# Kernel tuning notes

Measured on AMD Instinct MI355X. Metric: run time of the kernel, lower is better.

Reference implementation:

```python
import math
import jax, jax.numpy as jnp
import numpy as np

B, C, H, W = 8, 512, 32, 32
N_HEADS = 8
N_GROUPS = 32  # GroupNorm(32) as in guided-diffusion normalization()
EPS = 1e-5


def setup_inputs() -> dict:
    key = jax.random.key(0)
    k0, k1, k2, k3, k4 = jax.random.split(key, 5)
    x = jax.random.normal(k0, (B, C, H, W), dtype=jnp.float32)
    gn_scale = jnp.ones((C,), dtype=jnp.float32)
    gn_bias = jnp.zeros((C,), dtype=jnp.float32)
    # 1x1 conv weights stored as (out, in); proj_out is zero-initialized in the
    # original but we use small random weights so the op is non-trivial.
    qkv_w = jax.random.normal(k1, (3 * C, C), dtype=jnp.float32) * 0.02
    qkv_b = jax.random.normal(k2, (3 * C,), dtype=jnp.float32) * 0.02
    proj_w = jax.random.normal(k3, (C, C), dtype=jnp.float32) * 0.02
    proj_b = jax.random.normal(k4, (C,), dtype=jnp.float32) * 0.02
    return {"x": x, "gn_scale": gn_scale, "gn_bias": gn_bias,
            "qkv_w": qkv_w, "qkv_b": qkv_b, "proj_w": proj_w, "proj_b": proj_b}


def reference(x, gn_scale, gn_bias, qkv_w, qkv_b, proj_w, proj_b):
    b, c, h, w = x.shape
    L = h * w
    xf = x.reshape(b, c, L)

    # GroupNorm(32): normalize over (channels-in-group, length)
    xg = xf.reshape(b, N_GROUPS, c // N_GROUPS, L)
    mu = jnp.mean(xg, axis=(2, 3), keepdims=True)
    var = jnp.var(xg, axis=(2, 3), keepdims=True)
    xn = ((xg - mu) * jax.lax.rsqrt(var + EPS)).reshape(b, c, L)
    xn = xn * gn_scale[None, :, None] + gn_bias[None, :, None]

    # 1x1 conv -> qkv (b, 3c, L)
    qkv = jnp.einsum('oc,bcl->bol', qkv_w, xn) + qkv_b[None, :, None]

    ch = c // N_HEADS  # head dim (width//(3*n_heads) of qkv)
    q, k, v = jnp.split(qkv, 3, axis=1)
    q = q.reshape(b * N_HEADS, ch, L)
    k = k.reshape(b * N_HEADS, ch, L)
    v = v.reshape(b * N_HEADS, ch, L)

    scale = 1.0 / math.sqrt(math.sqrt(ch))
    # scores: (b*heads, L, L) materialized, as in the original
    wts = jnp.einsum('bct,bcs->bts', q * scale, k * scale)
    wts = jax.nn.softmax(wts.astype(jnp.float32), axis=-1).astype(q.dtype)
    a = jnp.einsum('bts,bcs->bct', wts, v).reshape(b, c, L)

    # zero-initialized 1x1 proj in original; random weights here
    hout = jnp.einsum('oc,bcl->bol', proj_w, a) + proj_b[None, :, None]
    return (xf + hout).reshape(b, c, h, w)
```

## Files before the change

kernel.cpp:

```cpp
#include <hip/hip_runtime.h>
#include <math.h>

#define BATCH   8
#define CCH     512
#define LL      1024
#define NHEADS  8
#define CHD     64
#define EPSV    1e-5f
#define QSCALE  0.1803368801111204f

typedef __bf16 bf16_t;
typedef bf16_t bf16x8 __attribute__((ext_vector_type(8)));
typedef bf16_t bf16x4 __attribute__((ext_vector_type(4)));
typedef float  f32x4  __attribute__((ext_vector_type(4)));

__device__ __forceinline__ bf16_t f2b(float f) {
  unsigned u = __float_as_uint(f);
  u += 0x7fff + ((u >> 16) & 1);
  return __builtin_bit_cast(bf16_t, (unsigned short)(u >> 16));
}

__device__ __forceinline__ unsigned pack2(float lo, float hi) {
  unsigned a = (unsigned)__builtin_bit_cast(unsigned short, f2b(lo));
  unsigned b = (unsigned)__builtin_bit_cast(unsigned short, f2b(hi));
  return (b << 16) | a;
}

__device__ __forceinline__ void gload_lds16(const void* g, void* l) {
  __builtin_amdgcn_global_load_lds(
      (const __attribute__((address_space(1))) void*)g,
      (__attribute__((address_space(3))) void*)l, 16, 0, 0);
}

__global__ __launch_bounds__(256) void prep_fused(const float* __restrict__ qkvw,
                                                  const float* __restrict__ projw,
                                                  bf16_t* __restrict__ wqb,
                                                  bf16_t* __restrict__ wpb,
                                                  const float* __restrict__ x,
                                                  const float* __restrict__ gsc,
                                                  const float* __restrict__ gbi,
                                                  bf16_t* __restrict__ xnT) {
  int bid = blockIdx.x;
  int tid = threadIdx.x;
  if (bid < 1024) {
    int i = (bid * 256 + tid) * 4;
    const float* src;
    bf16_t* dst;
    int j;
    if (i < 1536 * 512) { src = qkvw; dst = wqb; j = i; }
    else                { src = projw; dst = wpb; j = i - 1536 * 512; }
    float4 v = *(const float4*)(src + j);
    bf16x4 o = {f2b(v.x), f2b(v.y), f2b(v.z), f2b(v.w)};
    *(bf16x4*)(dst + j) = o;
    return;
  }
  int lin = bid - 1024;
  int xcd = lin & 7, slot = lin >> 3;
  int b = slot & 7, jj = slot >> 3;
  int g = xcd * 4 + jj;
  const float4* x4 = (const float4*)(x + ((size_t)(b * 32 + g)) * 16 * LL);

  float s = 0.f, ss = 0.f;
  float4 v[16];
#pragma unroll
  for (int it = 0; it < 16; ++it) {
    float4 f = x4[it * 256 + tid];
    v[it] = f;
    s += f.x + f.y + f.z + f.w;
    ss += f.x * f.x + f.y * f.y + f.z * f.z + f.w * f.w;
  }
#pragma unroll
  for (int m = 1; m < 64; m <<= 1) { s += __shfl_xor(s, m); ss += __shfl_xor(ss, m); }
  __shared__ float rs_[4], rss[4];
  int wv = tid >> 6, ln = tid & 63;
  if (ln == 0) { rs_[wv] = s; rss[wv] = ss; }
  __syncthreads();
  s  = rs_[0] + rs_[1] + rs_[2] + rs_[3];
  ss = rss[0] + rss[1] + rss[2] + rss[3];
  float mean = s * (1.f / 16384.f);
  float var  = ss * (1.f / 16384.f) - mean * mean;
  float rstd = rsqrtf(var + EPSV);

  float sc[16], bi[16];
#pragma unroll
  for (int it = 0; it < 16; ++it) {
    sc[it] = gsc[g * 16 + it] * rstd;
    bi[it] = gbi[g * 16 + it] - mean * sc[it];
  }

#pragma unroll
  for (int j = 0; j < 4; ++j) {
    unsigned w[8];
#pragma unroll
    for (int k = 0; k < 8; ++k) {
      float a0 = (j == 0 ? v[2 * k].x : j == 1 ? v[2 * k].y : j == 2 ? v[2 * k].z : v[2 * k].w);
      float a1 = (j == 0 ? v[2 * k + 1].x : j == 1 ? v[2 * k + 1].y : j == 2 ? v[2 * k + 1].z : v[2 * k + 1].w);
      w[k] = pack2(a0 * sc[2 * k] + bi[2 * k], a1 * sc[2 * k + 1] + bi[2 * k + 1]);
    }
    int l = tid * 4 + j;
    bf16_t* dst = xnT + ((size_t)b * LL + l) * CCH + g * 16;
    *(uint4*)dst = make_uint4(w[0], w[1], w[2], w[3]);
    *(uint4*)(dst + 8) = make_uint4(w[4], w[5], w[6], w[7]);
  }
}

__global__ __launch_bounds__(256, 2) void qkv_mfma(const bf16_t* __restrict__ wq,
                                                   const bf16_t* __restrict__ xnT,
                                                   const float* __restrict__ qkvb,
                                                   bf16_t* __restrict__ qt,
                                                   bf16_t* __restrict__ kt,
                                                   bf16_t* __restrict__ vt) {
  __shared__ bf16_t As[128 * 64];
  __shared__ bf16_t Bs[256 * 64];
  int tid = threadIdx.x;
  int wave = tid >> 6, lane = tid & 63;
  int lrow = lane & 15, quad = lane >> 4;
  int wm = wave >> 1, wn = wave & 1;
  int b = blockIdx.x;
  int oBase = blockIdx.y * 128, lBase = blockIdx.z * 256;
  int srow = lane >> 3;
  int sgOff = (((lane & 7) ^ srow) << 4);

  f32x4 acc[4][8] = {};
  for (int ktile = 0; ktile < 8; ++ktile) {
    int kB = ktile * 64;
    __syncthreads();
#pragma unroll
    for (int j = 0; j < 4; ++j) {
      int ci = wave * 4 + j;
      int R = ci * 8 + srow;
      gload_lds16((const char*)(wq + (size_t)(oBase + R) * CCH + kB) + sgOff,
                  (char*)As + ci * 1024);
    }
#pragma unroll
    for (int j = 0; j < 8; ++j) {
      int ci = wave * 8 + j;
      int R = ci * 8 + srow;
      gload_lds16((const char*)(xnT + ((size_t)b * LL + lBase + R) * CCH + kB) + sgOff,
                  (char*)Bs + ci * 1024);
    }
    __syncthreads();
#pragma unroll
    for (int kk = 0; kk < 2; ++kk) {
      int g = (kk * 4 + quad) ^ (lrow & 7);
      bf16x8 af[4], bfr[8];
#pragma unroll
      for (int m = 0; m < 4; ++m) {
        int r = wm * 64 + m * 16 + lrow;
        af[m] = *(const bf16x8*)(As + r * 64 + g * 8);
      }
#pragma unroll
      for (int n = 0; n < 8; ++n) {
        int r = wn * 128 + n * 16 + lrow;
        bfr[n] = *(const bf16x8*)(Bs + r * 64 + g * 8);
      }
#pragma unroll
      for (int m = 0; m < 4; ++m)
#pragma unroll
        for (int n = 0; n < 8; ++n)
          acc[m][n] = __builtin_amdgcn_mfma_f32_16x16x32_bf16(af[m], bfr[n], acc[m][n], 0, 0, 0);
    }
  }

  int oW = oBase + wm * 64;
  int lW = lBase + wn * 128;
  int sec = oW >> 9;
#pragma unroll
  for (int m = 0; m < 4; ++m) {
    int o4 = oW + m * 16 + quad * 4;
    float4 bb4 = *(const float4*)&qkvb[o4];
    int cc = o4 & 511;
    int head = cc >> 6, ch = cc & 63;
    int bh = b * NHEADS + head;
    if (sec == 0) {
#pragma unroll
      for (int n = 0; n < 8; ++n) {
        int l = lW + n * 16 + lrow;
        unsigned d0 = pack2((acc[m][n][0] + bb4.x) * QSCALE,
                            (acc[m][n][1] + bb4.y) * QSCALE);
        unsigned d1 = pack2((acc[m][n][2] + bb4.z) * QSCALE,
                            (acc[m][n][3] + bb4.w) * QSCALE);
        *(uint2*)(qt + ((size_t)bh * LL + l) * CHD + ch) = make_uint2(d0, d1);
      }
    } else if (sec == 1) {
#pragma unroll
      for (int n = 0; n < 8; ++n) {
        int l = lW + n * 16 + lrow;
        unsigned d0 = pack2(acc[m][n][0] + bb4.x, acc[m][n][1] + bb4.y);
        unsigned d1 = pack2(acc[m][n][2] + bb4.z, acc[m][n][3] + bb4.w);
        *(uint2*)(kt + ((size_t)bh * LL + l) * CHD + ch) = make_uint2(d0, d1);
      }
    } else {
      float bb[4] = {bb4.x, bb4.y, bb4.z, bb4.w};
#pragma unroll
      for (int c = 0; c < 2; ++c) {
#pragma unroll
        for (int i = 0; i < 4; ++i) {
          unsigned d0 = pack2(acc[m][c * 4 + 0][i] + bb[i], acc[m][c * 4 + 1][i] + bb[i]);
          unsigned d1 = pack2(acc[m][c * 4 + 2][i] + bb[i], acc[m][c * 4 + 3][i] + bb[i]);
          *(uint2*)(vt + ((size_t)bh * CHD + ch + i) * LL + lW + c * 64 + lrow * 4) =
              make_uint2(d0, d1);
        }
      }
    }
  }
}

__global__ __launch_bounds__(256) void attn_mfma(const bf16_t* __restrict__ qt,
                                                 const bf16_t* __restrict__ kt,
                                                 const bf16_t* __restrict__ vt,
                                                 bf16_t* __restrict__ at) {
  __shared__ bf16_t kbuf[2][64 * 64];
  __shared__ bf16_t vbuf[2][64 * 64];
  __shared__ bf16_t pb[8 * 16 * 72];
  int tid = threadIdx.x, wave = tid >> 6, lane = tid & 63;
  int lrow = lane & 15, quad = lane >> 4;
  int bh = blockIdx.x;
  int tW = blockIdx.y * 128 + wave * 32;
  const bf16_t* qb = qt + (size_t)bh * LL * CHD;
  const bf16_t* kb = kt + (size_t)bh * LL * CHD;
  const bf16_t* vb = vt + (size_t)bh * CHD * LL;

  int srow = lane >> 3;
  int sgb = (((lane & 7) ^ srow) << 4);

  bf16x8 qf[2][2];
#pragma unroll
  for (int h = 0; h < 2; ++h) {
    const bf16_t* qp = qb + (size_t)(tW + h * 16 + lrow) * CHD + quad * 8;
    qf[h][0] = *(const bf16x8*)qp;
    qf[h][1] = *(const bf16x8*)(qp + 32);
  }

  bf16x8 ones;
#pragma unroll
  for (int j = 0; j < 8; ++j) ones[j] = (bf16_t)1.0f;

  f32x4 Oa[2][4] = {};
  f32x4 Os[2] = {};

#pragma unroll
  for (int j = 0; j < 2; ++j) {
    int c = wave * 2 + j;
    int R = c * 8 + srow;
    gload_lds16((const char*)(kb + (size_t)R * CHD) + sgb, (char*)&kbuf[0][0] + c * 1024);
    gload_lds16((const char*)(vb + (size_t)R * LL) + sgb, (char*)&vbuf[0][0] + c * 1024);
  }
  __syncthreads();

  int swz0 = (quad ^ (lrow & 7)) * 8;
  int swz1 = ((quad + 4) ^ (lrow & 7)) * 8;

  for (int st = 0; st < 16; ++st) {
    int cur = st & 1;
    if (st < 15) {
      int sBn = (st + 1) * 64;
#pragma unroll
      for (int j = 0; j < 2; ++j) {
        int c = wave * 2 + j;
        int R = c * 8 + srow;
        gload_lds16((const char*)(kb + (size_t)(sBn + R) * CHD) + sgb,
                    (char*)&kbuf[cur ^ 1][0] + c * 1024);
        gload_lds16((const char*)(vb + (size_t)R * LL + sBn) + sgb,
                    (char*)&vbuf[cur ^ 1][0] + c * 1024);
      }
    }
    const bf16_t* kbase = &kbuf[cur][0];
    const bf16_t* vbase = &vbuf[cur][0];

    f32x4 S[2][4];
#pragma unroll
    for (int ss = 0; ss < 4; ++ss) {
      int s = ss * 16 + lrow;
      bf16x8 k0 = *(const bf16x8*)(kbase + s * 64 + swz0);
      bf16x8 k1 = *(const bf16x8*)(kbase + s * 64 + swz1);
#pragma unroll
      for (int h = 0; h < 2; ++h) {
        f32x4 z = {0.f, 0.f, 0.f, 0.f};
        z = __builtin_amdgcn_mfma_f32_16x16x32_bf16(qf[h][0], k0, z, 0, 0, 0);
        S[h][ss] = __builtin_amdgcn_mfma_f32_16x16x32_bf16(qf[h][1], k1, z, 0, 0, 0);
      }
    }

#pragma unroll
    for (int h = 0; h < 2; ++h) {
      bf16_t* pw = pb + (wave * 2 + h) * (16 * 72);
      float p[4][4];
#pragma unroll
      for (int ss = 0; ss < 4; ++ss)
#pragma unroll
        for (int i = 0; i < 4; ++i)
          p[ss][i] = __builtin_amdgcn_exp2f(S[h][ss][i]);
#pragma unroll
      for (int i = 0; i < 4; ++i) {
        unsigned d0 = __builtin_amdgcn_perm(__float_as_uint(p[1][i]),
                                            __float_as_uint(p[0][i]), 0x07060302u);
        unsigned d1 = __builtin_amdgcn_perm(__float_as_uint(p[3][i]),
                                            __float_as_uint(p[2][i]), 0x07060302u);
        uint2* dst = (uint2*)(pw + (quad * 4 + i) * 72 + lrow * 4);
        *dst = make_uint2(d0, d1);
      }
    }
    asm volatile("s_waitcnt lgkmcnt(0)" ::: "memory");

    bf16x8 pf[2][2];
#pragma unroll
    for (int h = 0; h < 2; ++h) {
      const bf16_t* pw = pb + (wave * 2 + h) * (16 * 72);
      pf[h][0] = *(const bf16x8*)(pw + lrow * 72 + quad * 8);
      pf[h][1] = *(const bf16x8*)(pw + lrow * 72 + 32 + quad * 8);
    }

#pragma unroll
    for (int n = 0; n < 4; ++n) {
      int r = (n * 16 + lrow) * 64;
      bf16x8 v0 = *(const bf16x8*)(vbase + r + swz0);
      bf16x8 v1 = *(const bf16x8*)(vbase + r + swz1);
#pragma unroll
      for (int h = 0; h < 2; ++h) {
        Oa[h][n] = __builtin_amdgcn_mfma_f32_16x16x32_bf16(pf[h][0], v0, Oa[h][n], 0, 0, 0);
        Oa[h][n] = __builtin_amdgcn_mfma_f32_16x16x32_bf16(pf[h][1], v1, Oa[h][n], 0, 0, 0);
      }
    }
#pragma unroll
    for (int h = 0; h < 2; ++h) {
      Os[h] = __builtin_amdgcn_mfma_f32_16x16x32_bf16(pf[h][0], ones, Os[h], 0, 0, 0);
      Os[h] = __builtin_amdgcn_mfma_f32_16x16x32_bf16(pf[h][1], ones, Os[h], 0, 0, 0);
    }

    __syncthreads();
  }

  bf16_t* ab = at + (size_t)bh * LL * CHD;
#pragma unroll
  for (int h = 0; h < 2; ++h) {
    float inv[4];
#pragma unroll
    for (int i = 0; i < 4; ++i) inv[i] = 1.f / Os[h][i];
#pragma unroll
    for (int n = 0; n < 4; ++n)
#pragma unroll
      for (int i = 0; i < 4; ++i)
        ab[(size_t)(tW + h * 16 + quad * 4 + i) * CHD + n * 16 + lrow] =
            f2b(Oa[h][n][i] * inv[i]);
  }
}

__global__ __launch_bounds__(256) void proj_mfma(const bf16_t* __restrict__ wp,
                                                 const bf16_t* __restrict__ at,
                                                 const float* __restrict__ projb,
                                                 const float* __restrict__ x,
                                                 float* __restrict__ out) {
  __shared__ bf16_t As[128 * 64];
  __shared__ bf16_t Bs[128 * 64];
  int tid = threadIdx.x;
  int wave = tid >> 6, lane = tid & 63;
  int lrow = lane & 15, quad = lane >> 4;
  int wm = wave >> 1, wn = wave & 1;
  int b = blockIdx.x;
  int oBase = blockIdx.y * 128, lBase = blockIdx.z * 128;
  int srow = lane >> 3;
  int sgOff = (((lane & 7) ^ srow) << 4);

  f32x4 acc[4][4] = {};
  for (int ktile = 0; ktile < 8; ++ktile) {
    int kB = ktile * 64;
    __syncthreads();
#pragma unroll
    for (int j = 0; j < 4; ++j) {
      int ci = wave * 4 + j;
      int R = ci * 8 + srow;
      gload_lds16((const char*)(wp + (size_t)(oBase + R) * CCH + kB) + sgOff,
                  (char*)As + ci * 1024);
      gload_lds16((const char*)(at + ((size_t)(b * NHEADS + ktile) * LL + lBase + R) * CHD) + sgOff,
                  (char*)Bs + ci * 1024);
    }
    __syncthreads();
#pragma unroll
    for (int kk = 0; kk < 2; ++kk) {
      int g = (kk * 4 + quad) ^ (lrow & 7);
      bf16x8 af[4], bfr[4];
#pragma unroll
      for (int m = 0; m < 4; ++m) {
        int r = wm * 64 + m * 16 + lrow;
        af[m] = *(const bf16x8*)(As + r * 64 + g * 8);
      }
#pragma unroll
      for (int n = 0; n < 4; ++n) {
        int r = wn * 64 + n * 16 + lrow;
        bfr[n] = *(const bf16x8*)(Bs + r * 64 + g * 8);
      }
#pragma unroll
      for (int m = 0; m < 4; ++m)
#pragma unroll
        for (int n = 0; n < 4; ++n)
          acc[m][n] = __builtin_amdgcn_mfma_f32_16x16x32_bf16(af[m], bfr[n], acc[m][n], 0, 0, 0);
    }
  }

  int oW = oBase + wm * 64;
  int lW = lBase + wn * 64;
#pragma unroll
  for (int m = 0; m < 4; ++m) {
#pragma unroll
    for (int i = 0; i < 4; ++i) {
      int o = oW + m * 16 + quad * 4 + i;
      float bb = projb[o];
#pragma unroll
      for (int n = 0; n < 4; ++n) {
        int l = lW + n * 16 + lrow;
        size_t off = ((size_t)(b * CCH + o)) * LL + l;
        out[off] = acc[m][n][i] + bb + x[off];
      }
    }
  }
}

extern "C" void kernel_launch(void* const* d_in, const int* in_sizes, int n_in,
                              void* d_out, int out_size, void* d_ws, size_t ws_size,
                              hipStream_t stream) {
  const float* x     = (const float*)d_in[0];
  const float* gsc   = (const float*)d_in[1];
  const float* gbi   = (const float*)d_in[2];
  const float* qkvw  = (const float*)d_in[3];
  const float* qkvb  = (const float*)d_in[4];
  const float* projw = (const float*)d_in[5];
  const float* projb = (const float*)d_in[6];
  float* out = (float*)d_out;

  char* ws = (char*)d_ws;
  bf16_t* wqb   = (bf16_t*)(ws + 4096);
  bf16_t* wpb   = (bf16_t*)(ws + 4096 + 1572864);
  bf16_t* xnT   = (bf16_t*)(ws + 2101248);
  bf16_t* qt    = (bf16_t*)(ws + 2101248 + 8388608);
  bf16_t* kt    = (bf16_t*)(ws + 2101248 + 2 * 8388608);
  bf16_t* vt    = (bf16_t*)(ws + 2101248 + 3 * 8388608);
  bf16_t* at    = (bf16_t*)(ws + 2101248 + 4 * 8388608);

  hipLaunchKernelGGL(prep_fused, dim3(1280), dim3(256), 0, stream,
                     qkvw, projw, wqb, wpb, x, gsc, gbi, xnT);
  hipLaunchKernelGGL(qkv_mfma, dim3(BATCH, 12, 4), dim3(256), 0, stream,
                     wqb, xnT, qkvb, qt, kt, vt);
  hipLaunchKernelGGL(attn_mfma, dim3(64, 8), dim3(256), 0, stream, qt, kt, vt, at);
  hipLaunchKernelGGL(proj_mfma, dim3(BATCH, 4, 8), dim3(256), 0, stream,
                     wpb, at, projb, x, out);
}
```

Before: 155.3 us.

## Double query rows per wave in attention and swizzle P tile in LDS

Measured after the change: 157.8 us. About the same (+1.6%).

```diff
diff --git a/kernel.cpp b/kernel.cpp
--- a/kernel.cpp
+++ b/kernel.cpp
@@ -206,17 +206,17 @@
   }
 }
 
-__global__ __launch_bounds__(256) void attn_mfma(const bf16_t* __restrict__ qt,
-                                                 const bf16_t* __restrict__ kt,
-                                                 const bf16_t* __restrict__ vt,
-                                                 bf16_t* __restrict__ at) {
+__global__ __launch_bounds__(256, 1) void attn_mfma(const bf16_t* __restrict__ qt,
+                                                    const bf16_t* __restrict__ kt,
+                                                    const bf16_t* __restrict__ vt,
+                                                    bf16_t* __restrict__ at) {
   __shared__ bf16_t kbuf[2][64 * 64];
   __shared__ bf16_t vbuf[2][64 * 64];
-  __shared__ bf16_t pb[8 * 16 * 72];
+  __shared__ bf16_t pb[4 * 4 * 16 * 64];
   int tid = threadIdx.x, wave = tid >> 6, lane = tid & 63;
   int lrow = lane & 15, quad = lane >> 4;
   int bh = blockIdx.x;
-  int tW = blockIdx.y * 128 + wave * 32;
+  int tW = blockIdx.y * 256 + wave * 64;
   const bf16_t* qb = qt + (size_t)bh * LL * CHD;
   const bf16_t* kb = kt + (size_t)bh * LL * CHD;
   const bf16_t* vb = vt + (size_t)bh * CHD * LL;
@@ -224,9 +224,9 @@
   int srow = lane >> 3;
   int sgb = (((lane & 7) ^ srow) << 4);
 
-  bf16x8 qf[2][2];
-#pragma unroll
-  for (int h = 0; h < 2; ++h) {
+  bf16x8 qf[4][2];
+#pragma unroll
+  for (int h = 0; h < 4; ++h) {
     const bf16_t* qp = qb + (size_t)(tW + h * 16 + lrow) * CHD + quad * 8;
     qf[h][0] = *(const bf16x8*)qp;
     qf[h][1] = *(const bf16x8*)(qp + 32);
@@ -236,8 +236,8 @@
 #pragma unroll
   for (int j = 0; j < 8; ++j) ones[j] = (bf16_t)1.0f;
 
-  f32x4 Oa[2][4] = {};
-  f32x4 Os[2] = {};
+  f32x4 Oa[4][4] = {};
+  f32x4 Os[4] = {};
 
 #pragma unroll
   for (int j = 0; j < 2; ++j) {
@@ -268,47 +268,49 @@
     const bf16_t* kbase = &kbuf[cur][0];
     const bf16_t* vbase = &vbuf[cur][0];
 
-    f32x4 S[2][4];
+    bf16x8 kf0[4], kf1[4];
 #pragma unroll
     for (int ss = 0; ss < 4; ++ss) {
       int s = ss * 16 + lrow;
-      bf16x8 k0 = *(const bf16x8*)(kbase + s * 64 + swz0);
-      bf16x8 k1 = *(const bf16x8*)(kbase + s * 64 + swz1);
-#pragma unroll
-      for (int h = 0; h < 2; ++h) {
+      kf0[ss] = *(const bf16x8*)(kbase + s * 64 + swz0);
+      kf1[ss] = *(const bf16x8*)(kbase + s * 64 + swz1);
+    }
+
+#pragma unroll
+    for (int h = 0; h < 4; ++h) {
+      f32x4 S[4];
+#pragma unroll
+      for (int ss = 0; ss < 4; ++ss) {
         f32x4 z = {0.f, 0.f, 0.f, 0.f};
-        z = __builtin_amdgcn_mfma_f32_16x16x32_bf16(qf[h][0], k0, z, 0, 0, 0);
-        S[h][ss] = __builtin_amdgcn_mfma_f32_16x16x32_bf16(qf[h][1], k1, z, 0, 0, 0);
-      }
-    }
-
-#pragma unroll
-    for (int h = 0; h < 2; ++h) {
-      bf16_t* pw = pb + (wave * 2 + h) * (16 * 72);
+        z = __builtin_amdgcn_mfma_f32_16x16x32_bf16(qf[h][0], kf0[ss], z, 0, 0, 0);
+        S[ss] = __builtin_amdgcn_mfma_f32_16x16x32_bf16(qf[h][1], kf1[ss], z, 0, 0, 0);
+      }
       float p[4][4];
 #pragma unroll
       for (int ss = 0; ss < 4; ++ss)
 #pragma unroll
         for (int i = 0; i < 4; ++i)
-          p[ss][i] = __builtin_amdgcn_exp2f(S[h][ss][i]);
+          p[ss][i] = __builtin_amdgcn_exp2f(S[ss][i]);
+      bf16_t* pw = pb + (wave * 4 + h) * 1024;
 #pragma unroll
       for (int i = 0; i < 4; ++i) {
+        int t = quad * 4 + i;
         unsigned d0 = __builtin_amdgcn_perm(__float_as_uint(p[1][i]),
                                             __float_as_uint(p[0][i]), 0x07060302u);
         unsigned d1 = __builtin_amdgcn_perm(__float_as_uint(p[3][i]),
                                             __float_as_uint(p[2][i]), 0x07060302u);
-        uint2* dst = (uint2*)(pw + (quad * 4 + i) * 72 + lrow * 4);
-        *dst = make_uint2(d0, d1);
+        int off = t * 64 + ((((lrow >> 1) ^ (t & 7)) << 3) | ((lrow & 1) << 2));
+        *(uint2*)(pw + off) = make_uint2(d0, d1);
       }
     }
     asm volatile("s_waitcnt lgkmcnt(0)" ::: "memory");
 
-    bf16x8 pf[2][2];
-#pragma unroll
-    for (int h = 0; h < 2; ++h) {
-      const bf16_t* pw = pb + (wave * 2 + h) * (16 * 72);
-      pf[h][0] = *(const bf16x8*)(pw + lrow * 72 + quad * 8);
-      pf[h][1] = *(const bf16x8*)(pw + lrow * 72 + 32 + quad * 8);
+    bf16x8 pf0[4], pf1[4];
+#pragma unroll
+    for (int h = 0; h < 4; ++h) {
+      const bf16_t* pw = pb + (wave * 4 + h) * 1024;
+      pf0[h] = *(const bf16x8*)(pw + lrow * 64 + swz0);
+      pf1[h] = *(const bf16x8*)(pw + lrow * 64 + swz1);
     }
 
 #pragma unroll
@@ -317,15 +319,15 @@
       bf16x8 v0 = *(const bf16x8*)(vbase + r + swz0);
       bf16x8 v1 = *(const bf16x8*)(vbase + r + swz1);
 #pragma unroll
-      for (int h = 0; h < 2; ++h) {
-        Oa[h][n] = __builtin_amdgcn_mfma_f32_16x16x32_bf16(pf[h][0], v0, Oa[h][n], 0, 0, 0);
-        Oa[h][n] = __builtin_amdgcn_mfma_f32_16x16x32_bf16(pf[h][1], v1, Oa[h][n], 0, 0, 0);
-      }
-    }
-#pragma unroll
-    for (int h = 0; h < 2; ++h) {
-      Os[h] = __builtin_amdgcn_mfma_f32_16x16x32_bf16(pf[h][0], ones, Os[h], 0, 0, 0);
-      Os[h] = __builtin_amdgcn_mfma_f32_16x16x32_bf16(pf[h][1], ones, Os[h], 0, 0, 0);
+      for (int h = 0; h < 4; ++h) {
+        Oa[h][n] = __builtin_amdgcn_mfma_f32_16x16x32_bf16(pf0[h], v0, Oa[h][n], 0, 0, 0);
+        Oa[h][n] = __builtin_amdgcn_mfma_f32_16x16x32_bf16(pf1[h], v1, Oa[h][n], 0, 0, 0);
+      }
+    }
+#pragma unroll
+    for (int h = 0; h < 4; ++h) {
+      Os[h] = __builtin_amdgcn_mfma_f32_16x16x32_bf16(pf0[h], ones, Os[h], 0, 0, 0);
+      Os[h] = __builtin_amdgcn_mfma_f32_16x16x32_bf16(pf1[h], ones, Os[h], 0, 0, 0);
     }
 
     __syncthreads();
@@ -333,7 +335,7 @@
 
   bf16_t* ab = at + (size_t)bh * LL * CHD;
 #pragma unroll
-  for (int h = 0; h < 2; ++h) {
+  for (int h = 0; h < 4; ++h) {
     float inv[4];
 #pragma unroll
     for (int i = 0; i < 4; ++i) inv[i] = 1.f / Os[h][i];
@@ -441,7 +443,7 @@
                      qkvw, projw, wqb, wpb, x, gsc, gbi, xnT);
   hipLaunchKernelGGL(qkv_mfma, dim3(BATCH, 12, 4), dim3(256), 0, stream,
                      wqb, xnT, qkvb, qt, kt, vt);
-  hipLaunchKernelGGL(attn_mfma, dim3(64, 8), dim3(256), 0, stream, qt, kt, vt, at);
+  hipLaunchKernelGGL(attn_mfma, dim3(64, 4), dim3(256), 0, stream, qt, kt, vt, at);
   hipLaunchKernelGGL(proj_mfma, dim3(BATCH, 4, 8), dim3(256), 0, stream,
                      wpb, at, projb, x, out);
 }
```
